# Performance work log

Measured on AMD Instinct MI355X. Metric: run time of the kernel, lower is better.

Reference implementation:

```python
import jax, jax.numpy as jnp
import numpy as np

D_IN = 1024
D_OUT = 1024
NUM_HEADS = 16
HEAD_DIM = D_OUT // NUM_HEADS


def setup_inputs() -> dict:
    key = jax.random.key(0)
    ks = jax.random.split(key, 6)
    B, S = 2, 2048
    x = jax.random.normal(ks[0], (B, S, D_IN), dtype=jnp.float32)
    # nn.Linear stores weight as [out, in]; y = x @ W.T
    scale_in = 1.0 / np.sqrt(D_IN)
    w_query = jax.random.uniform(ks[1], (D_OUT, D_IN), jnp.float32, -scale_in, scale_in)
    w_key = jax.random.uniform(ks[2], (D_OUT, D_IN), jnp.float32, -scale_in, scale_in)
    w_value = jax.random.uniform(ks[3], (D_OUT, D_IN), jnp.float32, -scale_in, scale_in)
    scale_out = 1.0 / np.sqrt(D_OUT)
    w_out = jax.random.uniform(ks[4], (D_OUT, D_OUT), jnp.float32, -scale_out, scale_out)
    b_out = jax.random.uniform(ks[5], (D_OUT,), jnp.float32, -scale_out, scale_out)
    return {"x": x, "w_query": w_query, "w_key": w_key, "w_value": w_value,
            "w_out": w_out, "b_out": b_out}


def reference(x, w_query, w_key, w_value, w_out, b_out):
    B, S, _ = x.shape
    H, Dh = NUM_HEADS, HEAD_DIM
    # projections (no qkv bias), split heads -> [B, H, S, Dh]
    q = (x @ w_query.T).reshape(B, S, H, Dh).transpose(0, 2, 1, 3)
    k = (x @ w_key.T).reshape(B, S, H, Dh).transpose(0, 2, 1, 3)
    v = (x @ w_value.T).reshape(B, S, H, Dh).transpose(0, 2, 1, 3)
    # explicit [B, H, S, S] scores with causal mask (matches masked_fill(triu,-inf))
    scores = jnp.einsum('bhqd,bhkd->bhqk', q, k)
    causal = jnp.tril(jnp.ones((S, S), dtype=bool))  # True = keep
    scores = jnp.where(causal, scores, -jnp.inf)
    attn = jax.nn.softmax(scores / np.sqrt(Dh).astype(np.float32), axis=-1)
    # dropout p=0.0 -> identity
    ctx = jnp.einsum('bhqk,bhkd->bhqd', attn, v)  # [B, H, S, Dh]
    ctx = ctx.transpose(0, 2, 1, 3).reshape(B, S, H * Dh)
    return ctx @ w_out.T + b_out
```

## Files before the change

kernel.cpp:

```cpp
#include <hip/hip_runtime.h>
#include <hip/hip_bf16.h>

typedef __attribute__((ext_vector_type(8))) short short8;
typedef __attribute__((ext_vector_type(4))) short short4_t;
typedef __attribute__((ext_vector_type(8))) float f32x8;
typedef __attribute__((ext_vector_type(4))) float f32x4;

#define MFMA16(a, b, c) __builtin_amdgcn_mfma_f32_16x16x32_bf16((a), (b), (c), 0, 0, 0)


static __device__ __forceinline__ short f2bf(float f) {
    __hip_bfloat16 h = __float2bfloat16(f);
    return *reinterpret_cast<short*>(&h);
}

static __device__ __forceinline__ unsigned pack2bf(float lo, float hi) {
    return ((unsigned)f2bf(lo) & 0xffffu) | ((unsigned)f2bf(hi) << 16);
}

static __device__ __forceinline__ void g2l16(const void* g, void* l) {
    __builtin_amdgcn_global_load_lds(
        (const __attribute__((address_space(1))) void*)g,
        (__attribute__((address_space(3))) void*)l,
        16, 0, 0);
}

__global__ __launch_bounds__(256) void cvt_kernel(
    const float* __restrict__ x,  const float* __restrict__ wq,
    const float* __restrict__ wk, const float* __restrict__ wv,
    const float* __restrict__ wo, __hip_bfloat16* __restrict__ ws)
{
    const size_t e = ((size_t)blockIdx.x * 256 + threadIdx.x) * 8;
    const float* src;
    __hip_bfloat16* dst;
    size_t off;
    if (e < 4194304)      { src = x;  dst = ws + 16777216; off = e; }
    else if (e < 5242880) { src = wq; dst = ws + 20971520; off = e - 4194304; }
    else if (e < 6291456) { src = wk; dst = ws + 20971520 + 1048576; off = e - 5242880; }
    else if (e < 7340032) { src = wv; dst = ws + 20971520 + 2097152; off = e - 6291456; }
    else                  { src = wo; dst = ws + 24117248; off = e - 7340032; }

    f32x8 v = *reinterpret_cast<const f32x8*>(src + off);
    short8 o;
#pragma unroll
    for (int j = 0; j < 8; ++j) o[j] = f2bf(v[j]);
    *reinterpret_cast<short8*>(reinterpret_cast<short*>(dst) + off) = o;
}

__global__ __launch_bounds__(256) void qkv_gemm_kernel(
    const __hip_bfloat16* __restrict__ xbf_,
    const __hip_bfloat16* __restrict__ wqkv_,
    __hip_bfloat16* __restrict__ qkv_out)
{
    const int bid = blockIdx.x;
    const int xcd = bid & 7, kb = bid >> 3;
    const int mBlk = xcd * 4 + (kb / 24);
    const int nBlk = kb % 24;

    const int tid  = threadIdx.x;
    const int lane = tid & 63;
    const int wid  = tid >> 6;
    const int l16  = lane & 15;
    const int lhi  = lane >> 4;
    const int wr = wid >> 1, wc = wid & 1;

    const short* A = reinterpret_cast<const short*>(xbf_);
    const short* Bm = reinterpret_cast<const short*>(wqkv_);
    const int r0A = mBlk * 128, r0B = nBlk * 128;

    __shared__ __align__(16) short sA[128 * 64];
    __shared__ __align__(16) short sB[128 * 64];

    f32x4 acc[4][4] = {};

    for (int kk = 0; kk < 1024; kk += 64) {
#pragma unroll
        for (int it = 0; it < 4; ++it) {
            const int G = it * 256 + tid;
            const int row = G >> 3, gs = G & 7;
            const int gl = gs ^ (row & 7);
            short* lp = sA + (size_t)(it * 256 + wid * 64) * 8;
            g2l16(A + (size_t)(r0A + row) * 1024 + kk + gl * 8, lp);
        }
#pragma unroll
        for (int it = 0; it < 4; ++it) {
            const int G = it * 256 + tid;
            const int row = G >> 3, gs = G & 7;
            const int gl = gs ^ (row & 7);
            short* lp = sB + (size_t)(it * 256 + wid * 64) * 8;
            g2l16(Bm + (size_t)(r0B + row) * 1024 + kk + gl * 8, lp);
        }
        __syncthreads();

#pragma unroll
        for (int ks = 0; ks < 2; ++ks) {
            short8 a[4], b[4];
#pragma unroll
            for (int i = 0; i < 4; ++i) {
                const int row = wr * 64 + i * 16 + l16;
                const int sg = (ks * 4 + lhi) ^ (row & 7);
                a[i] = *reinterpret_cast<const short8*>(&sA[row * 64 + sg * 8]);
            }
#pragma unroll
            for (int j = 0; j < 4; ++j) {
                const int row = wc * 64 + j * 16 + l16;
                const int sg = (ks * 4 + lhi) ^ (row & 7);
                b[j] = *reinterpret_cast<const short8*>(&sB[row * 64 + sg * 8]);
            }
#pragma unroll
            for (int i = 0; i < 4; ++i)
#pragma unroll
                for (int j = 0; j < 4; ++j)
                    acc[i][j] = MFMA16(a[i], b[j], acc[i][j]);
        }
        __syncthreads();
    }

    const int nTileBase = nBlk * 128 + wc * 64;
    const int mat = (nTileBase >> 10);
    __hip_bfloat16* dst = qkv_out + (size_t)mat * 4194304;
    const int mBase = r0A + wr * 64;

    if (mat < 2) {
        const float qscl = (mat == 0) ? 0.18033688f : 1.0f;
#pragma unroll
        for (int i = 0; i < 4; ++i)
#pragma unroll
            for (int j = 0; j < 4; ++j)
#pragma unroll
                for (int r = 0; r < 4; ++r) {
                    const int mRow = mBase + i * 16 + lhi * 4 + r;
                    const int nCol = (nTileBase + j * 16 + l16) & 1023;
                    const int bb = mRow >> 11, s = mRow & 2047;
                    const int h = nCol >> 6, d = nCol & 63;
                    dst[(((size_t)(bb * 16 + h) * 2048 + s) << 6) + d] =
                        __float2bfloat16(acc[i][j][r] * qscl);
                }
    } else {
#pragma unroll
        for (int i = 0; i < 4; ++i) {
            const int mRow0 = mBase + i * 16 + lhi * 4;
            const int bb = mRow0 >> 11, s0 = mRow0 & 2047;
#pragma unroll
            for (int j = 0; j < 4; ++j) {
                const int nCol = (nTileBase + j * 16 + l16) & 1023;
                const int h = nCol >> 6, d = nCol & 63;
                short4_t v4;
#pragma unroll
                for (int r = 0; r < 4; ++r) v4[r] = f2bf(acc[i][j][r]);
                *reinterpret_cast<short4_t*>(
                    reinterpret_cast<short*>(dst) +
                    (((size_t)(bb * 16 + h) * 64 + d) << 11) + s0) = v4;
            }
        }
    }
}

__global__ __launch_bounds__(512, 4) void attn_kernel(
    const __hip_bfloat16* __restrict__ qkv,
    __hip_bfloat16* __restrict__ ctx)
{
    const int tid  = threadIdx.x;
    const int lane = tid & 63;
    const int wid  = tid >> 6;
    const int l16 = lane & 15;
    const int lhi = lane >> 4;

    const int bid = blockIdx.x;
    const int xcd = bid & 7, idx = bid >> 3;
    const int h4 = idx & 3, tg = idx >> 2;
    const int bh = xcd * 4 + h4;
    const int g  = (tg < 8) ? (15 - tg) : (tg - 8);
    const int qt = g * 8 + wid;
    const int q0 = qt * 16;
    const int sd = q0 >> 6;
    const int ns_blk = 2 * g + 2;

    const short* Q  = reinterpret_cast<const short*>(qkv) + (size_t)bh * 131072;
    const short* K  = Q + 4194304;
    const short* Vt = Q + 8388608;

    __shared__ __align__(16) short sK[2][64 * 64];
    __shared__ __align__(16) short sV[2][64 * 64];
    __shared__ __align__(16) short p_lds_all[8][16 * 72];
    short* p_lds = p_lds_all[wid];

    const int bb = bh >> 4, h = bh & 15;

    short8 qf[2];
    qf[0] = *reinterpret_cast<const short8*>(Q + (size_t)(q0 + l16) * 64 + lhi * 8);
    qf[1] = *reinterpret_cast<const short8*>(Q + (size_t)(q0 + l16) * 64 + 32 + lhi * 8);

    f32x4 oacc[4] = {};
    float lsum = 0.0f;

    const int srow = tid >> 3, sgs = tid & 7;
    const int sgl = sgs ^ (srow & 7);
    auto stage = [&](int buf, int kv0) {
        g2l16(K + (size_t)(kv0 + srow) * 64 + sgl * 8, &sK[buf][(size_t)tid * 8]);
        g2l16(Vt + (size_t)srow * 2048 + kv0 + sgl * 8, &sV[buf][(size_t)tid * 8]);
    };

    stage(0, 0);
    asm volatile("s_waitcnt vmcnt(0)" ::: "memory");
    __syncthreads();

    const int r7 = l16 & 7;
    int cur = 0;
#pragma unroll 1
    for (int st = 0; st < ns_blk; ++st) {
        const int kv0 = st * 64;
        if (st + 1 < ns_blk) stage(cur ^ 1, kv0 + 64);

        if (st <= sd) {
            f32x4 sc[4];
#pragma unroll
            for (int nt = 0; nt < 4; ++nt) {
                f32x4 s = {};
#pragma unroll
                for (int ks = 0; ks < 2; ++ks) {
                    const int sg = (ks * 4 + lhi) ^ r7;
                    short8 kb = *reinterpret_cast<const short8*>(
                        &sK[cur][(nt * 16 + l16) * 64 + sg * 8]);
                    s = MFMA16(kb, qf[ks], s);
                }
                sc[nt] = s;
            }

            if (st == sd) {
#pragma unroll
                for (int nt = 0; nt < 4; ++nt) {
                    const int kvb = kv0 + nt * 16 + lhi * 4;
                    const int qrow = q0 + l16;
#pragma unroll
                    for (int r = 0; r < 4; ++r)
                        if (kvb + r > qrow) sc[nt][r] = -1.0e38f;
                }
            }
#pragma unroll
            for (int nt = 0; nt < 4; ++nt) {
                const float p0 = exp2f(sc[nt][0]);
                const float p1 = exp2f(sc[nt][1]);
                const float p2 = exp2f(sc[nt][2]);
                const float p3 = exp2f(sc[nt][3]);
                lsum += (p0 + p1) + (p2 + p3);
                uint2 w;
                w.x = pack2bf(p0, p1);
                w.y = pack2bf(p2, p3);
                *reinterpret_cast<uint2*>(&p_lds[l16 * 72 + nt * 16 + lhi * 4]) = w;
            }
            asm volatile("s_waitcnt lgkmcnt(0)" ::: "memory");

#pragma unroll
            for (int ks = 0; ks < 2; ++ks) {
                short8 pf = *reinterpret_cast<const short8*>(
                    &p_lds[l16 * 72 + ks * 32 + lhi * 8]);
#pragma unroll
                for (int dt = 0; dt < 4; ++dt) {
                    const int sg = (ks * 4 + lhi) ^ r7;
                    short8 vb = *reinterpret_cast<const short8*>(
                        &sV[cur][(dt * 16 + l16) * 64 + sg * 8]);
                    oacc[dt] = MFMA16(pf, vb, oacc[dt]);
                }
            }
        }

        asm volatile("s_waitcnt vmcnt(0)" ::: "memory");
        __syncthreads();
        cur ^= 1;
    }

    float rs = lsum;
    rs += __shfl_xor(rs, 16);
    rs += __shfl_xor(rs, 32);
    const float rinvq = 1.0f / rs;
    float rinv[4];
#pragma unroll
    for (int r = 0; r < 4; ++r) rinv[r] = __shfl(rinvq, lhi * 4 + r);

#pragma unroll
    for (int dt = 0; dt < 4; ++dt)
#pragma unroll
        for (int r = 0; r < 4; ++r) {
            const int q = q0 + lhi * 4 + r;
            ctx[((size_t)bb * 2048 + q) * 1024 + h * 64 + dt * 16 + l16] =
                __float2bfloat16(oacc[dt][r] * rinv[r]);
        }
}

__global__ __launch_bounds__(256) void out_gemm_kernel(
    const __hip_bfloat16* __restrict__ ctx,
    const __hip_bfloat16* __restrict__ wobf,
    const float* __restrict__ bo,
    float* __restrict__ out)
{
    const int bid = blockIdx.x;
    const int xcd = bid & 7, kb = bid >> 3;
    const int mBlk = xcd * 4 + (kb >> 3);
    const int nBlk = kb & 7;

    const int tid  = threadIdx.x;
    const int lane = tid & 63;
    const int wid  = tid >> 6;
    const int l16  = lane & 15;
    const int lhi  = lane >> 4;
    const int wr = wid >> 1, wc = wid & 1;

    const short* A = reinterpret_cast<const short*>(ctx);
    const short* Bm = reinterpret_cast<const short*>(wobf);
    const int r0A = mBlk * 128, r0B = nBlk * 128;

    __shared__ __align__(16) short sA[128 * 64];
    __shared__ __align__(16) short sB[128 * 64];

    f32x4 acc[4][4] = {};

    for (int kk = 0; kk < 1024; kk += 64) {
#pragma unroll
        for (int it = 0; it < 4; ++it) {
            const int G = it * 256 + tid;
            const int row = G >> 3, gs = G & 7;
            const int gl = gs ^ (row & 7);
            short* lp = sA + (size_t)(it * 256 + wid * 64) * 8;
            g2l16(A + (size_t)(r0A + row) * 1024 + kk + gl * 8, lp);
        }
#pragma unroll
        for (int it = 0; it < 4; ++it) {
            const int G = it * 256 + tid;
            const int row = G >> 3, gs = G & 7;
            const int gl = gs ^ (row & 7);
            short* lp = sB + (size_t)(it * 256 + wid * 64) * 8;
            g2l16(Bm + (size_t)(r0B + row) * 1024 + kk + gl * 8, lp);
        }
        __syncthreads();

#pragma unroll
        for (int ks = 0; ks < 2; ++ks) {
            short8 a[4], b[4];
#pragma unroll
            for (int i = 0; i < 4; ++i) {
                const int row = wr * 64 + i * 16 + l16;
                const int sg = (ks * 4 + lhi) ^ (row & 7);
                a[i] = *reinterpret_cast<const short8*>(&sA[row * 64 + sg * 8]);
            }
#pragma unroll
            for (int j = 0; j < 4; ++j) {
                const int row = wc * 64 + j * 16 + l16;
                const int sg = (ks * 4 + lhi) ^ (row & 7);
                b[j] = *reinterpret_cast<const short8*>(&sB[row * 64 + sg * 8]);
            }
#pragma unroll
            for (int i = 0; i < 4; ++i)
#pragma unroll
                for (int j = 0; j < 4; ++j)
                    acc[i][j] = MFMA16(a[i], b[j], acc[i][j]);
        }
        __syncthreads();
    }

    const int mBase = r0A + wr * 64;
    const int nBase = r0B + wc * 64;
#pragma unroll
    for (int i = 0; i < 4; ++i)
#pragma unroll
        for (int j = 0; j < 4; ++j)
#pragma unroll
            for (int r = 0; r < 4; ++r) {
                const int mRow = mBase + i * 16 + lhi * 4 + r;
                const int nCol = nBase + j * 16 + l16;
                out[(size_t)mRow * 1024 + nCol] = acc[i][j][r] + bo[nCol];
            }
}

extern "C" void kernel_launch(void* const* d_in, const int* in_sizes, int n_in,
                              void* d_out, int out_size, void* d_ws, size_t ws_size,
                              hipStream_t stream) {
    const float* x  = (const float*)d_in[0];
    const float* wq = (const float*)d_in[1];
    const float* wk = (const float*)d_in[2];
    const float* wv = (const float*)d_in[3];
    const float* wo = (const float*)d_in[4];
    const float* bo = (const float*)d_in[5];

    __hip_bfloat16* ws = (__hip_bfloat16*)d_ws;
    __hip_bfloat16* ctx  = ws + 12582912;
    __hip_bfloat16* xbf  = ws + 16777216;
    __hip_bfloat16* wqkv = ws + 20971520;
    __hip_bfloat16* wobf = ws + 24117248;
    float* out = (float*)d_out;

    cvt_kernel<<<4096, 256, 0, stream>>>(x, wq, wk, wv, wo, ws);
    qkv_gemm_kernel<<<768, 256, 0, stream>>>(xbf, wqkv, ws);
    attn_kernel<<<512, 512, 0, stream>>>(ws, ctx);
    out_gemm_kernel<<<256, 256, 0, stream>>>(ctx, wobf, bo, out);
}
```

Before: 118.2 us.

## Switch attention to 32x32 MFMA tiles and feed P through registers

Each attention wave now handles 32 query rows with 32x32x16 bf16 MFMAs instead of 16 rows with 16x16x32, and blocks shrink to 4 waves. The exp'd probabilities are packed straight into MFMA A-operands in registers, which removes the per-wave LDS round-trip and its wait. Each K/V tile staged into LDS is reused across more query rows per wave. The cost is more accumulator registers per wave, fewer waves per block, and V reads split into two 8-byte LDS loads per fragment.

Measured after the change: 129.8 us. +9.8%, slower.

```diff
diff --git a/kernel.cpp b/kernel.cpp
--- a/kernel.cpp
+++ b/kernel.cpp
@@ -5,8 +5,12 @@
 typedef __attribute__((ext_vector_type(4))) short short4_t;
 typedef __attribute__((ext_vector_type(8))) float f32x8;
 typedef __attribute__((ext_vector_type(4))) float f32x4;
+typedef __attribute__((ext_vector_type(16))) float f32x16;
+typedef __attribute__((ext_vector_type(2))) unsigned uint2v;
+typedef __attribute__((ext_vector_type(4))) unsigned uint4v;
 
 #define MFMA16(a, b, c) __builtin_amdgcn_mfma_f32_16x16x32_bf16((a), (b), (c), 0, 0, 0)
+#define MFMA32(a, b, c) __builtin_amdgcn_mfma_f32_32x32x16_bf16((a), (b), (c), 0, 0, 0)
 
 
 static __device__ __forceinline__ short f2bf(float f) {
@@ -16,6 +20,12 @@
 
 static __device__ __forceinline__ unsigned pack2bf(float lo, float hi) {
     return ((unsigned)f2bf(lo) & 0xffffu) | ((unsigned)f2bf(hi) << 16);
+}
+
+static __device__ __forceinline__ short8 u4_to_s8(uint4v u) {
+    short8 s;
+    __builtin_memcpy(&s, &u, 16);
+    return s;
 }
 
 static __device__ __forceinline__ void g2l16(const void* g, void* l) {
@@ -156,24 +166,24 @@
     }
 }
 
-__global__ __launch_bounds__(512, 4) void attn_kernel(
+__global__ __launch_bounds__(256) void attn_kernel(
     const __hip_bfloat16* __restrict__ qkv,
     __hip_bfloat16* __restrict__ ctx)
 {
     const int tid  = threadIdx.x;
     const int lane = tid & 63;
     const int wid  = tid >> 6;
-    const int l16 = lane & 15;
-    const int lhi = lane >> 4;
+    const int l32  = lane & 31;
+    const int hi2  = lane >> 5;
 
     const int bid = blockIdx.x;
     const int xcd = bid & 7, idx = bid >> 3;
     const int h4 = idx & 3, tg = idx >> 2;
     const int bh = xcd * 4 + h4;
     const int g  = (tg < 8) ? (15 - tg) : (tg - 8);
-    const int qt = g * 8 + wid;
-    const int q0 = qt * 16;
-    const int sd = q0 >> 6;
+    const int qt = g * 4 + wid;
+    const int q0 = qt * 32;
+    const int sd = (q0 + 31) >> 6;
     const int ns_blk = 2 * g + 2;
 
     const short* Q  = reinterpret_cast<const short*>(qkv) + (size_t)bh * 131072;
@@ -182,30 +192,35 @@
 
     __shared__ __align__(16) short sK[2][64 * 64];
     __shared__ __align__(16) short sV[2][64 * 64];
-    __shared__ __align__(16) short p_lds_all[8][16 * 72];
-    short* p_lds = p_lds_all[wid];
 
     const int bb = bh >> 4, h = bh & 15;
-
-    short8 qf[2];
-    qf[0] = *reinterpret_cast<const short8*>(Q + (size_t)(q0 + l16) * 64 + lhi * 8);
-    qf[1] = *reinterpret_cast<const short8*>(Q + (size_t)(q0 + l16) * 64 + 32 + lhi * 8);
-
-    f32x4 oacc[4] = {};
+    const int qrow = q0 + l32;
+    const int r7 = l32 & 7;
+
+    short8 qf[4];
+#pragma unroll
+    for (int kc = 0; kc < 4; ++kc)
+        qf[kc] = *reinterpret_cast<const short8*>(
+            Q + (size_t)qrow * 64 + kc * 16 + hi2 * 8);
+
+    f32x16 oacc[2] = {};
     float lsum = 0.0f;
 
-    const int srow = tid >> 3, sgs = tid & 7;
-    const int sgl = sgs ^ (srow & 7);
     auto stage = [&](int buf, int kv0) {
-        g2l16(K + (size_t)(kv0 + srow) * 64 + sgl * 8, &sK[buf][(size_t)tid * 8]);
-        g2l16(Vt + (size_t)srow * 2048 + kv0 + sgl * 8, &sV[buf][(size_t)tid * 8]);
+#pragma unroll
+        for (int it = 0; it < 2; ++it) {
+            const int G = it * 256 + tid;
+            const int row = G >> 3, gs = G & 7;
+            const int gl = gs ^ (row & 7);
+            g2l16(K + (size_t)(kv0 + row) * 64 + gl * 8, &sK[buf][(size_t)G * 8]);
+            g2l16(Vt + (size_t)row * 2048 + kv0 + gl * 8, &sV[buf][(size_t)G * 8]);
+        }
     };
 
     stage(0, 0);
     asm volatile("s_waitcnt vmcnt(0)" ::: "memory");
     __syncthreads();
 
-    const int r7 = l16 & 7;
     int cur = 0;
 #pragma unroll 1
     for (int st = 0; st < ns_blk; ++st) {
@@ -213,54 +228,68 @@
         if (st + 1 < ns_blk) stage(cur ^ 1, kv0 + 64);
 
         if (st <= sd) {
-            f32x4 sc[4];
-#pragma unroll
-            for (int nt = 0; nt < 4; ++nt) {
-                f32x4 s = {};
-#pragma unroll
-                for (int ks = 0; ks < 2; ++ks) {
-                    const int sg = (ks * 4 + lhi) ^ r7;
+            f32x16 sc[2];
+#pragma unroll
+            for (int t = 0; t < 2; ++t) {
+                f32x16 s = {};
+#pragma unroll
+                for (int kc = 0; kc < 4; ++kc) {
+                    const int row = t * 32 + l32;
+                    const int sg = (kc * 2 + hi2) ^ r7;
                     short8 kb = *reinterpret_cast<const short8*>(
-                        &sK[cur][(nt * 16 + l16) * 64 + sg * 8]);
-                    s = MFMA16(kb, qf[ks], s);
+                        &sK[cur][row * 64 + sg * 8]);
+                    s = MFMA32(kb, qf[kc], s);
                 }
-                sc[nt] = s;
+                sc[t] = s;
             }
 
             if (st == sd) {
 #pragma unroll
-                for (int nt = 0; nt < 4; ++nt) {
-                    const int kvb = kv0 + nt * 16 + lhi * 4;
-                    const int qrow = q0 + l16;
-#pragma unroll
-                    for (int r = 0; r < 4; ++r)
-                        if (kvb + r > qrow) sc[nt][r] = -1.0e38f;
+                for (int t = 0; t < 2; ++t)
+#pragma unroll
+                    for (int r = 0; r < 16; ++r) {
+                        const int kv = kv0 + t * 32 + (r & 3) + 8 * (r >> 2) + 4 * hi2;
+                        if (kv > qrow) sc[t][r] = -1.0e38f;
+                    }
+            }
+
+            unsigned pkt[2][8];
+#pragma unroll
+            for (int t = 0; t < 2; ++t) {
+                float pv[16];
+#pragma unroll
+                for (int r = 0; r < 16; ++r) {
+                    pv[r] = exp2f(sc[t][r]);
+                    lsum += pv[r];
                 }
-            }
-#pragma unroll
-            for (int nt = 0; nt < 4; ++nt) {
-                const float p0 = exp2f(sc[nt][0]);
-                const float p1 = exp2f(sc[nt][1]);
-                const float p2 = exp2f(sc[nt][2]);
-                const float p3 = exp2f(sc[nt][3]);
-                lsum += (p0 + p1) + (p2 + p3);
-                uint2 w;
-                w.x = pack2bf(p0, p1);
-                w.y = pack2bf(p2, p3);
-                *reinterpret_cast<uint2*>(&p_lds[l16 * 72 + nt * 16 + lhi * 4]) = w;
-            }
-            asm volatile("s_waitcnt lgkmcnt(0)" ::: "memory");
-
-#pragma unroll
-            for (int ks = 0; ks < 2; ++ks) {
-                short8 pf = *reinterpret_cast<const short8*>(
-                    &p_lds[l16 * 72 + ks * 32 + lhi * 8]);
-#pragma unroll
-                for (int dt = 0; dt < 4; ++dt) {
-                    const int sg = (ks * 4 + lhi) ^ r7;
-                    short8 vb = *reinterpret_cast<const short8*>(
-                        &sV[cur][(dt * 16 + l16) * 64 + sg * 8]);
-                    oacc[dt] = MFMA16(pf, vb, oacc[dt]);
+#pragma unroll
+                for (int i = 0; i < 8; ++i)
+                    pkt[t][i] = pack2bf(pv[2 * i], pv[2 * i + 1]);
+            }
+
+#pragma unroll
+            for (int ks4 = 0; ks4 < 4; ++ks4) {
+                const int t = ks4 >> 1;
+                const int b = (ks4 & 1) * 4;
+                uint4v up;
+                up[0] = pkt[t][b + 0];
+                up[1] = pkt[t][b + 1];
+                up[2] = pkt[t][b + 2];
+                up[3] = pkt[t][b + 3];
+                short8 pa = u4_to_s8(up);
+#pragma unroll
+                for (int dt = 0; dt < 2; ++dt) {
+                    const int row = dt * 32 + l32;
+                    const int g0 = (2 * ks4) ^ (row & 7);
+                    const int g1 = (2 * ks4 + 1) ^ (row & 7);
+                    const char* base = reinterpret_cast<const char*>(&sV[cur][row * 64]);
+                    uint2v lo  = *reinterpret_cast<const uint2v*>(base + g0 * 16 + hi2 * 8);
+                    uint2v hiw = *reinterpret_cast<const uint2v*>(base + g1 * 16 + hi2 * 8);
+                    uint4v uv;
+                    uv[0] = lo[0];  uv[1] = lo[1];
+                    uv[2] = hiw[0]; uv[3] = hiw[1];
+                    short8 vb = u4_to_s8(uv);
+                    oacc[dt] = MFMA32(pa, vb, oacc[dt]);
                 }
             }
         }
@@ -270,22 +299,19 @@
         cur ^= 1;
     }
 
-    float rs = lsum;
-    rs += __shfl_xor(rs, 16);
-    rs += __shfl_xor(rs, 32);
+    float rs = lsum + __shfl_xor(lsum, 32);
     const float rinvq = 1.0f / rs;
-    float rinv[4];
-#pragma unroll
-    for (int r = 0; r < 4; ++r) rinv[r] = __shfl(rinvq, lhi * 4 + r);
-
-#pragma unroll
-    for (int dt = 0; dt < 4; ++dt)
-#pragma unroll
-        for (int r = 0; r < 4; ++r) {
-            const int q = q0 + lhi * 4 + r;
-            ctx[((size_t)bb * 2048 + q) * 1024 + h * 64 + dt * 16 + l16] =
-                __float2bfloat16(oacc[dt][r] * rinv[r]);
-        }
+
+#pragma unroll
+    for (int r = 0; r < 16; ++r) {
+        const int qrl = (r & 3) + 8 * (r >> 2) + 4 * hi2;
+        const float rv = __shfl(rinvq, qrl);
+#pragma unroll
+        for (int dt = 0; dt < 2; ++dt) {
+            ctx[((size_t)bb * 2048 + q0 + qrl) * 1024 + h * 64 + dt * 32 + l32] =
+                __float2bfloat16(oacc[dt][r] * rv);
+        }
+    }
 }
 
 __global__ __launch_bounds__(256) void out_gemm_kernel(
@@ -391,6 +417,6 @@
 
     cvt_kernel<<<4096, 256, 0, stream>>>(x, wq, wk, wv, wo, ws);
     qkv_gemm_kernel<<<768, 256, 0, stream>>>(xbf, wqkv, ws);
-    attn_kernel<<<512, 512, 0, stream>>>(ws, ctx);
+    attn_kernel<<<512, 256, 0, stream>>>(ws, ctx);
     out_gemm_kernel<<<256, 256, 0, stream>>>(ctx, wobf, bo, out);
 }
```

## Keep P in registers and shrink attention blocks to four waves per query tile

Applied to the files above, without the earlier changes.

The attention kernel now keeps the softmax probabilities in registers and feeds them straight into the PV MFMA. It does this by permuting the K dimension consistently between P and V reads, which removes the per-wave LDS round trip and its waitcnt. Blocks shrink from 8 waves to 4, each covering 64 query rows, with twice as many blocks. Every block now processes exactly g+1 KV tiles with no idle skip branch. This cuts LDS traffic and wasted causal iterations, at the cost of each block loading K/V tiles for fewer query rows and V reads being split into 8-byte LDS loads.

Result: no change. 118.3 us (+0.1%).

```diff
diff --git a/kernel.cpp b/kernel.cpp
--- a/kernel.cpp
+++ b/kernel.cpp
@@ -5,6 +5,8 @@
 typedef __attribute__((ext_vector_type(4))) short short4_t;
 typedef __attribute__((ext_vector_type(8))) float f32x8;
 typedef __attribute__((ext_vector_type(4))) float f32x4;
+typedef __attribute__((ext_vector_type(2))) unsigned uint2v;
+typedef __attribute__((ext_vector_type(4))) unsigned uint4v;
 
 #define MFMA16(a, b, c) __builtin_amdgcn_mfma_f32_16x16x32_bf16((a), (b), (c), 0, 0, 0)
 
@@ -16,6 +18,12 @@
 
 static __device__ __forceinline__ unsigned pack2bf(float lo, float hi) {
     return ((unsigned)f2bf(lo) & 0xffffu) | ((unsigned)f2bf(hi) << 16);
+}
+
+static __device__ __forceinline__ short8 u4_to_s8(uint4v u) {
+    short8 s;
+    __builtin_memcpy(&s, &u, 16);
+    return s;
 }
 
 static __device__ __forceinline__ void g2l16(const void* g, void* l) {
@@ -156,7 +164,7 @@
     }
 }
 
-__global__ __launch_bounds__(512, 4) void attn_kernel(
+__global__ __launch_bounds__(256, 4) void attn_kernel(
     const __hip_bfloat16* __restrict__ qkv,
     __hip_bfloat16* __restrict__ ctx)
 {
@@ -170,11 +178,10 @@
     const int xcd = bid & 7, idx = bid >> 3;
     const int h4 = idx & 3, tg = idx >> 2;
     const int bh = xcd * 4 + h4;
-    const int g  = (tg < 8) ? (15 - tg) : (tg - 8);
-    const int qt = g * 8 + wid;
+    const int g  = (tg < 16) ? (31 - tg) : (tg - 16);
+    const int qt = g * 4 + wid;
     const int q0 = qt * 16;
-    const int sd = q0 >> 6;
-    const int ns_blk = 2 * g + 2;
+    const int ns_blk = g + 1;
 
     const short* Q  = reinterpret_cast<const short*>(qkv) + (size_t)bh * 131072;
     const short* K  = Q + 4194304;
@@ -182,86 +189,97 @@
 
     __shared__ __align__(16) short sK[2][64 * 64];
     __shared__ __align__(16) short sV[2][64 * 64];
-    __shared__ __align__(16) short p_lds_all[8][16 * 72];
-    short* p_lds = p_lds_all[wid];
 
     const int bb = bh >> 4, h = bh & 15;
+    const int qrow = q0 + l16;
+    const int r7 = l16 & 7;
 
     short8 qf[2];
-    qf[0] = *reinterpret_cast<const short8*>(Q + (size_t)(q0 + l16) * 64 + lhi * 8);
-    qf[1] = *reinterpret_cast<const short8*>(Q + (size_t)(q0 + l16) * 64 + 32 + lhi * 8);
+    qf[0] = *reinterpret_cast<const short8*>(Q + (size_t)qrow * 64 + lhi * 8);
+    qf[1] = *reinterpret_cast<const short8*>(Q + (size_t)qrow * 64 + 32 + lhi * 8);
 
     f32x4 oacc[4] = {};
     float lsum = 0.0f;
 
-    const int srow = tid >> 3, sgs = tid & 7;
-    const int sgl = sgs ^ (srow & 7);
     auto stage = [&](int buf, int kv0) {
-        g2l16(K + (size_t)(kv0 + srow) * 64 + sgl * 8, &sK[buf][(size_t)tid * 8]);
-        g2l16(Vt + (size_t)srow * 2048 + kv0 + sgl * 8, &sV[buf][(size_t)tid * 8]);
+#pragma unroll
+        for (int it = 0; it < 2; ++it) {
+            const int G = it * 256 + tid;
+            const int row = G >> 3, gs = G & 7;
+            const int gl = gs ^ (row & 7);
+            g2l16(K + (size_t)(kv0 + row) * 64 + gl * 8, &sK[buf][(size_t)G * 8]);
+            g2l16(Vt + (size_t)row * 2048 + kv0 + gl * 8, &sV[buf][(size_t)G * 8]);
+        }
     };
 
     stage(0, 0);
     asm volatile("s_waitcnt vmcnt(0)" ::: "memory");
     __syncthreads();
 
-    const int r7 = l16 & 7;
     int cur = 0;
 #pragma unroll 1
     for (int st = 0; st < ns_blk; ++st) {
         const int kv0 = st * 64;
         if (st + 1 < ns_blk) stage(cur ^ 1, kv0 + 64);
 
-        if (st <= sd) {
-            f32x4 sc[4];
+        f32x4 sc[4];
+#pragma unroll
+        for (int nt = 0; nt < 4; ++nt) {
+            f32x4 s = {};
+#pragma unroll
+            for (int ks = 0; ks < 2; ++ks) {
+                const int sg = (ks * 4 + lhi) ^ r7;
+                short8 kb = *reinterpret_cast<const short8*>(
+                    &sK[cur][(nt * 16 + l16) * 64 + sg * 8]);
+                s = MFMA16(kb, qf[ks], s);
+            }
+            sc[nt] = s;
+        }
+
+        if (st == ns_blk - 1) {
 #pragma unroll
             for (int nt = 0; nt < 4; ++nt) {
-                f32x4 s = {};
-#pragma unroll
-                for (int ks = 0; ks < 2; ++ks) {
-                    const int sg = (ks * 4 + lhi) ^ r7;
-                    short8 kb = *reinterpret_cast<const short8*>(
-                        &sK[cur][(nt * 16 + l16) * 64 + sg * 8]);
-                    s = MFMA16(kb, qf[ks], s);
-                }
-                sc[nt] = s;
-            }
-
-            if (st == sd) {
-#pragma unroll
-                for (int nt = 0; nt < 4; ++nt) {
-                    const int kvb = kv0 + nt * 16 + lhi * 4;
-                    const int qrow = q0 + l16;
-#pragma unroll
-                    for (int r = 0; r < 4; ++r)
-                        if (kvb + r > qrow) sc[nt][r] = -1.0e38f;
-                }
-            }
-#pragma unroll
-            for (int nt = 0; nt < 4; ++nt) {
-                const float p0 = exp2f(sc[nt][0]);
-                const float p1 = exp2f(sc[nt][1]);
-                const float p2 = exp2f(sc[nt][2]);
-                const float p3 = exp2f(sc[nt][3]);
-                lsum += (p0 + p1) + (p2 + p3);
-                uint2 w;
-                w.x = pack2bf(p0, p1);
-                w.y = pack2bf(p2, p3);
-                *reinterpret_cast<uint2*>(&p_lds[l16 * 72 + nt * 16 + lhi * 4]) = w;
-            }
-            asm volatile("s_waitcnt lgkmcnt(0)" ::: "memory");
-
-#pragma unroll
-            for (int ks = 0; ks < 2; ++ks) {
-                short8 pf = *reinterpret_cast<const short8*>(
-                    &p_lds[l16 * 72 + ks * 32 + lhi * 8]);
-#pragma unroll
-                for (int dt = 0; dt < 4; ++dt) {
-                    const int sg = (ks * 4 + lhi) ^ r7;
-                    short8 vb = *reinterpret_cast<const short8*>(
-                        &sV[cur][(dt * 16 + l16) * 64 + sg * 8]);
-                    oacc[dt] = MFMA16(pf, vb, oacc[dt]);
-                }
+                const int kvb = kv0 + nt * 16 + lhi * 4;
+#pragma unroll
+                for (int r = 0; r < 4; ++r)
+                    if (kvb + r > qrow) sc[nt][r] = -1.0e38f;
+            }
+        }
+
+        unsigned pw[4][2];
+#pragma unroll
+        for (int nt = 0; nt < 4; ++nt) {
+            const float p0 = exp2f(sc[nt][0]);
+            const float p1 = exp2f(sc[nt][1]);
+            const float p2 = exp2f(sc[nt][2]);
+            const float p3 = exp2f(sc[nt][3]);
+            lsum += (p0 + p1) + (p2 + p3);
+            pw[nt][0] = pack2bf(p0, p1);
+            pw[nt][1] = pack2bf(p2, p3);
+        }
+
+#pragma unroll
+        for (int ks = 0; ks < 2; ++ks) {
+            uint4v up;
+            up[0] = pw[2 * ks][0];
+            up[1] = pw[2 * ks][1];
+            up[2] = pw[2 * ks + 1][0];
+            up[3] = pw[2 * ks + 1][1];
+            short8 pa = u4_to_s8(up);
+#pragma unroll
+            for (int dt = 0; dt < 4; ++dt) {
+                const int row = dt * 16 + l16;
+                const int g0 = (ks * 4 + (lhi >> 1)) ^ (row & 7);
+                const int g1 = (ks * 4 + 2 + (lhi >> 1)) ^ (row & 7);
+                const int sub = (lhi & 1) * 8;
+                const char* base = reinterpret_cast<const char*>(&sV[cur][row * 64]);
+                uint2v lo  = *reinterpret_cast<const uint2v*>(base + g0 * 16 + sub);
+                uint2v hiw = *reinterpret_cast<const uint2v*>(base + g1 * 16 + sub);
+                uint4v uv;
+                uv[0] = lo[0];  uv[1] = lo[1];
+                uv[2] = hiw[0]; uv[3] = hiw[1];
+                short8 vb = u4_to_s8(uv);
+                oacc[dt] = MFMA16(pa, vb, oacc[dt]);
             }
         }
 
@@ -391,6 +409,6 @@
 
     cvt_kernel<<<4096, 256, 0, stream>>>(x, wq, wk, wv, wo, ws);
     qkv_gemm_kernel<<<768, 256, 0, stream>>>(xbf, wqkv, ws);
-    attn_kernel<<<512, 512, 0, stream>>>(ws, ctx);
+    attn_kernel<<<1024, 256, 0, stream>>>(ws, ctx);
     out_gemm_kernel<<<256, 256, 0, stream>>>(ctx, wobf, bo, out);
 }
```
